# Optimization experiments

Measured on AMD Instinct MI355X. Metric: run time of the kernel, lower is better.

## Reference

```python
import jax, jax.numpy as jnp
import numpy as np

NUM_HEADS = 16


def setup_inputs() -> dict:
    key = jax.random.key(0)
    ks = jax.random.split(key, 5)
    B, S, D = 2, 2048, 1024
    x = jax.random.normal(ks[0], (B, S, D), dtype=jnp.float32)
    # Linear weights stored torch-style as [out, in]; init scale ~ 1/sqrt(D)
    scale = 1.0 / np.sqrt(D)
    Wq = jax.random.uniform(ks[1], (D, D), jnp.float32, -scale, scale)
    bq = jax.random.uniform(ks[2], (D,), jnp.float32, -scale, scale)
    Wo = jax.random.uniform(ks[3], (D, D), jnp.float32, -scale, scale)
    bo = jax.random.uniform(ks[4], (D,), jnp.float32, -scale, scale)
    return {"x": x, "Wq": Wq, "bq": bq, "Wo": Wo, "bo": bo}


def reference(x, Wq, bq, Wo, bo):
    B, S, D = x.shape
    H = NUM_HEADS
    Hd = D // H
    # NOTE: faithful to the source bug — Q, K, V all use the *query* projection.
    q = x @ Wq.T + bq                       # [B,S,D]
    qh = q.reshape(B, S, H, Hd).transpose(0, 2, 1, 3)  # [B,H,S,Hd]
    scores = jnp.einsum('bhsd,bhtd->bhst', qh, qh) / jnp.sqrt(jnp.float32(Hd))
    weights = jax.nn.softmax(scores, axis=-1)          # [B,H,S,S]
    attn = jnp.einsum('bhst,bhtd->bhsd', weights, qh)  # [B,H,S,Hd]
    attn = attn.transpose(0, 2, 1, 3).reshape(B, S, D)
    return attn @ Wo.T + bo
```

## Files before the change

### kernel.cpp

```cpp
#include <hip/hip_runtime.h>
#include <hip/hip_bf16.h>

typedef __bf16 bf16x8 __attribute__((ext_vector_type(8)));
typedef float  f32x4  __attribute__((ext_vector_type(4)));
typedef float  f32x16 __attribute__((ext_vector_type(16)));

__device__ __forceinline__ void gload_lds16(const void* g, void* l) {
  __builtin_amdgcn_global_load_lds(
      (const __attribute__((address_space(1))) unsigned int*)g,
      (__attribute__((address_space(3))) unsigned int*)l, 16, 0, 0);
}

__device__ __forceinline__ void xcd_remap(int& x, int& y) {
  const int lin = blockIdx.x + (blockIdx.y << 4);
  const int xcd = lin & 7, slot = lin >> 3;
  y = ((slot >> 4) << 3) + xcd;
  x = slot & 15;
}

__global__ void k_cvt(const float* __restrict__ s, __bf16* __restrict__ d, int n4) {
  int i = blockIdx.x * blockDim.x + threadIdx.x;
  if (i >= n4) return;
  float4 v = ((const float4*)s)[i];
  union { __bf16 h[4]; uint2 u; } o;
  o.h[0] = (__bf16)v.x; o.h[1] = (__bf16)v.y;
  o.h[2] = (__bf16)v.z; o.h[3] = (__bf16)v.w;
  ((uint2*)d)[i] = o.u;
}

template<bool OUT_BF16>
__global__ __launch_bounds__(256, 2)
void k_gemm_bt(const __bf16* __restrict__ A, const __bf16* __restrict__ B,
               const float* __restrict__ bias, void* __restrict__ C,
               int M, int N, int K) {
  __shared__ __align__(16) __bf16 At[4][128 * 32];
  __shared__ __align__(16) __bf16 Bt[4][64 * 32];
  const int tid  = threadIdx.x;
  const int lane = tid & 63;
  const int w    = tid >> 6;
  const int wr   = w >> 1, wc = w & 1;
  int bx, by; xcd_remap(bx, by);
  const int bm = by * 128, bn = bx * 64;

  f32x4 acc[4][2] = {};

  const __bf16* ga = A + (size_t)(bm + (tid >> 2)) * K + (tid & 3) * 8;
  const __bf16* gb = B + (size_t)(bn + (tid >> 2)) * K + (tid & 3) * 8;

#pragma unroll
  for (int p = 0; p < 2; ++p) {
    gload_lds16(ga + p * 32,                  &At[p][(w * 16) * 32]);
    gload_lds16(ga + p * 32 + (size_t)64 * K, &At[p][(64 + w * 16) * 32]);
    gload_lds16(gb + p * 32,                  &Bt[p][(w * 16) * 32]);
  }

  const int NIT = K / 32;
  for (int it = 0; it < NIT; ++it) {
    const int cur = it & 3;
    if (it + 2 < NIT) {
      const int nb = (it + 2) & 3;
      const int k2 = (it + 2) * 32;
      gload_lds16(ga + k2,                  &At[nb][(w * 16) * 32]);
      gload_lds16(ga + k2 + (size_t)64 * K, &At[nb][(64 + w * 16) * 32]);
      gload_lds16(gb + k2,                  &Bt[nb][(w * 16) * 32]);
      asm volatile("s_waitcnt vmcnt(6)" ::: "memory");
    } else if (it + 2 == NIT) {
      asm volatile("s_waitcnt vmcnt(3)" ::: "memory");
    } else {
      asm volatile("s_waitcnt vmcnt(0)" ::: "memory");
    }
    __builtin_amdgcn_s_barrier();
    __builtin_amdgcn_sched_barrier(0);

    bf16x8 a[4], b[2];
#pragma unroll
    for (int mt = 0; mt < 4; ++mt)
      a[mt] = *(const bf16x8*)&At[cur][(wr * 64 + mt * 16 + (lane & 15)) * 32 + (lane >> 4) * 8];
#pragma unroll
    for (int nt = 0; nt < 2; ++nt)
      b[nt] = *(const bf16x8*)&Bt[cur][(wc * 32 + nt * 16 + (lane & 15)) * 32 + (lane >> 4) * 8];
    __builtin_amdgcn_s_setprio(1);
#pragma unroll
    for (int mt = 0; mt < 4; ++mt)
#pragma unroll
      for (int nt = 0; nt < 2; ++nt)
        acc[mt][nt] = __builtin_amdgcn_mfma_f32_16x16x32_bf16(a[mt], b[nt], acc[mt][nt], 0, 0, 0);
    __builtin_amdgcn_s_setprio(0);
  }

#pragma unroll
  for (int nt = 0; nt < 2; ++nt) {
    const int col = bn + wc * 32 + nt * 16 + (lane & 15);
    const float bv = bias[col];
#pragma unroll
    for (int mt = 0; mt < 4; ++mt) {
#pragma unroll
      for (int r = 0; r < 4; ++r) {
        const int row = bm + wr * 64 + mt * 16 + (lane >> 4) * 4 + r;
        const float v = acc[mt][nt][r] + bv;
        if (OUT_BF16) ((__bf16*)C)[(size_t)row * N + col] = (__bf16)v;
        else          ((float*)C)[(size_t)row * N + col]  = v;
      }
    }
  }
}

#define SWZ2(row, col) ((row) * 64 + ((col) ^ (((((row) & 7) ^ ((row) >> 3)) & 7) << 3)))

#define ATTN_TILE(T, KB, VB)                                                  \
  {                                                                           \
    *(bf16x8*)&KB[SWZ2(2 * sm, c0)]     = v0;                                 \
    *(bf16x8*)&KB[SWZ2(2 * sm + 1, c0)] = v1;                                 \
    _Pragma("unroll")                                                         \
    for (int j = 0; j < 8; ++j) {                                             \
      union { __bf16 b[2]; unsigned u; } pk;                                  \
      pk.b[0] = v0[j]; pk.b[1] = v1[j];                                       \
      *(unsigned*)&VB[SWZ2(c0 + j, 2 * sm)] = pk.u;                           \
    }                                                                         \
    __syncthreads();                                                          \
    if ((T) < 31) {                                                           \
      v0 = *(const bf16x8*)&gsrc[(size_t)((T) + 1) * 64 * 1024];              \
      v1 = *(const bf16x8*)&gsrc[(size_t)((T) + 1) * 64 * 1024 + 1024];       \
    }                                                                         \
    f32x16 s[2] = {};                                                         \
    _Pragma("unroll")                                                         \
    for (int kvf = 0; kvf < 2; ++kvf) {                                       \
      __builtin_amdgcn_s_setprio(1);                                          \
      _Pragma("unroll")                                                       \
      for (int ks = 0; ks < 4; ++ks) {                                        \
        bf16x8 ka = *(const bf16x8*)&KB[SWZ2(kvf * 32 + l31, ks * 16 + h * 8)]; \
        s[kvf] = __builtin_amdgcn_mfma_f32_32x32x16_bf16(ka, qb[ks], s[kvf], 0, 0, 0); \
      }                                                                       \
      __builtin_amdgcn_s_setprio(0);                                          \
    }                                                                         \
    float ls0 = 0.f, ls1 = 0.f, ls2 = 0.f, ls3 = 0.f;                         \
    unsigned P[2][4][2];                                                      \
    _Pragma("unroll")                                                         \
    for (int kvf = 0; kvf < 2; ++kvf) {                                       \
      _Pragma("unroll")                                                       \
      for (int rq = 0; rq < 4; ++rq) {                                        \
        _Pragma("unroll")                                                     \
        for (int tt = 0; tt < 2; ++tt) {                                      \
          const float p0 = __builtin_amdgcn_exp2f(s[kvf][rq * 4 + tt * 2]);   \
          const float p1 = __builtin_amdgcn_exp2f(s[kvf][rq * 4 + tt * 2 + 1]); \
          if (tt == 0) { ls0 += p0; ls1 += p1; } else { ls2 += p0; ls3 += p1; } \
          union { __bf16 b[2]; unsigned u; } pk;                              \
          pk.b[0] = (__bf16)p0; pk.b[1] = (__bf16)p1;                         \
          P[kvf][rq][tt] = pk.u;                                              \
        }                                                                     \
      }                                                                       \
    }                                                                         \
    float lsum = (ls0 + ls1) + (ls2 + ls3);                                   \
    lsum += __shfl_xor(lsum, 32);                                             \
    l_run += lsum;                                                            \
    _Pragma("unroll")                                                         \
    for (int ko = 0; ko < 4; ++ko) {                                          \
      const int kvf = ko >> 1, rqa = (ko & 1) * 2, rqb = rqa + 1;             \
      asm volatile("v_permlane32_swap_b32 %0, %1"                             \
                   : "+v"(P[kvf][rqa][0]), "+v"(P[kvf][rqb][0]));             \
      asm volatile("v_permlane32_swap_b32 %0, %1"                             \
                   : "+v"(P[kvf][rqa][1]), "+v"(P[kvf][rqb][1]));             \
    }                                                                         \
    _Pragma("unroll")                                                         \
    for (int dh = 0; dh < 2; ++dh) {                                          \
      __builtin_amdgcn_s_setprio(1);                                          \
      _Pragma("unroll")                                                       \
      for (int ko = 0; ko < 4; ++ko) {                                        \
        const int kvf = ko >> 1, rqa = (ko & 1) * 2, rqb = rqa + 1;           \
        union { unsigned u[4]; bf16x8 v; } pu;                                \
        pu.u[0] = P[kvf][rqa][0]; pu.u[1] = P[kvf][rqa][1];                   \
        pu.u[2] = P[kvf][rqb][0]; pu.u[3] = P[kvf][rqb][1];                   \
        bf16x8 vb = *(const bf16x8*)&VB[SWZ2(dh * 32 + l31, ko * 16 + h * 8)]; \
        O[dh] = __builtin_amdgcn_mfma_f32_32x32x16_bf16(pu.v, vb, O[dh], 0, 0, 0); \
      }                                                                       \
      __builtin_amdgcn_s_setprio(0);                                          \
    }                                                                         \
  }

__global__ __launch_bounds__(256, 2)
void k_attn(const __bf16* __restrict__ q, __bf16* __restrict__ o) {
  __shared__ __align__(16) __bf16 Kt[2][64 * 64];
  __shared__ __align__(16) __bf16 Vt[2][64 * 64];
  const int tid = threadIdx.x, lane = tid & 63;
  const int w = tid >> 6;
  const int l31 = lane & 31, h = lane >> 5;
  int bqx, bh; xcd_remap(bqx, bh);
  const size_t base = ((size_t)(bh >> 4) * 2048) * 1024 + (bh & 15) * 64;
  const int q0 = bqx * 128 + w * 32;
  const float c2 = 0.18033688f;

  bf16x8 qb[4];
#pragma unroll
  for (int ks = 0; ks < 4; ++ks) {
    union { bf16x8 v; __bf16 b[8]; } u;
    u.v = *(const bf16x8*)&q[base + (size_t)(q0 + l31) * 1024 + ks * 16 + h * 8];
#pragma unroll
    for (int j = 0; j < 8; ++j) u.b[j] = (__bf16)((float)u.b[j] * c2);
    qb[ks] = u.v;
  }

  f32x16 O[2] = {};
  float l_run = 0.f;

  const int sm = tid >> 3, c0 = (tid & 7) * 8;
  const __bf16* gsrc = q + base + (size_t)(2 * sm) * 1024 + c0;

  __bf16* const K0 = &Kt[0][0];  __bf16* const V0 = &Vt[0][0];
  __bf16* const K1 = &Kt[1][0];  __bf16* const V1 = &Vt[1][0];

  bf16x8 v0 = *(const bf16x8*)&gsrc[0];
  bf16x8 v1 = *(const bf16x8*)&gsrc[1024];

  for (int t2 = 0; t2 < 16; ++t2) {
    ATTN_TILE(2 * t2,     K0, V0)
    ATTN_TILE(2 * t2 + 1, K1, V1)
  }

  const float linv = 1.0f / l_run;
#pragma unroll
  for (int r = 0; r < 16; ++r) {
    const int qrow = (r & 3) + 8 * (r >> 2) + 4 * h;
    const float rs = __shfl(linv, qrow);
    o[base + (size_t)(q0 + qrow) * 1024 + l31]      = (__bf16)(O[0][r] * rs);
    o[base + (size_t)(q0 + qrow) * 1024 + 32 + l31] = (__bf16)(O[1][r] * rs);
  }
}

extern "C" void kernel_launch(void* const* d_in, const int* in_sizes, int n_in,
                              void* d_out, int out_size, void* d_ws, size_t ws_size,
                              hipStream_t stream) {
  const float* x  = (const float*)d_in[0];
  const float* Wq = (const float*)d_in[1];
  const float* bq = (const float*)d_in[2];
  const float* Wo = (const float*)d_in[3];
  const float* bo = (const float*)d_in[4];

  char* ws = (char*)d_ws;
  __bf16* xb  = (__bf16*)(ws);
  __bf16* ab  = (__bf16*)(ws);
  __bf16* wqb = (__bf16*)(ws + ((size_t)8  << 20));
  __bf16* wob = (__bf16*)(ws + ((size_t)10 << 20));
  __bf16* qb  = (__bf16*)(ws + ((size_t)12 << 20));

  const int M = 4096, N = 1024, K = 1024;

  k_cvt<<<(M * K / 4 + 255) / 256, 256, 0, stream>>>(x,  xb,  M * K / 4);
  k_cvt<<<(N * K / 4 + 255) / 256, 256, 0, stream>>>(Wq, wqb, N * K / 4);
  k_cvt<<<(N * K / 4 + 255) / 256, 256, 0, stream>>>(Wo, wob, N * K / 4);

  k_gemm_bt<true ><<<dim3(16, 32), 256, 0, stream>>>(xb, wqb, bq, qb, M, N, K);
  k_attn          <<<dim3(16, 32), 256, 0, stream>>>(qb, ab);
  k_gemm_bt<false><<<dim3(16, 32), 256, 0, stream>>>(ab, wob, bo, d_out, M, N, K);
}
```

Before: 97.95 us.

## Split attention KV range across two blocks with merge kernel; deepen GEMM k-step

New measurement: 104.0 us. 1.06x slower.

```diff
diff --git a/kernel.cpp b/kernel.cpp
--- a/kernel.cpp
+++ b/kernel.cpp
@@ -33,8 +33,8 @@
 void k_gemm_bt(const __bf16* __restrict__ A, const __bf16* __restrict__ B,
                const float* __restrict__ bias, void* __restrict__ C,
                int M, int N, int K) {
-  __shared__ __align__(16) __bf16 At[4][128 * 32];
-  __shared__ __align__(16) __bf16 Bt[4][64 * 32];
+  __shared__ __align__(16) __bf16 At[3][2][128 * 32];
+  __shared__ __align__(16) __bf16 Bt[3][2][64 * 32];
   const int tid  = threadIdx.x;
   const int lane = tid & 63;
   const int w    = tid >> 6;
@@ -47,46 +47,56 @@
   const __bf16* ga = A + (size_t)(bm + (tid >> 2)) * K + (tid & 3) * 8;
   const __bf16* gb = B + (size_t)(bn + (tid >> 2)) * K + (tid & 3) * 8;
 
-#pragma unroll
-  for (int p = 0; p < 2; ++p) {
-    gload_lds16(ga + p * 32,                  &At[p][(w * 16) * 32]);
-    gload_lds16(ga + p * 32 + (size_t)64 * K, &At[p][(64 + w * 16) * 32]);
-    gload_lds16(gb + p * 32,                  &Bt[p][(w * 16) * 32]);
-  }
-
-  const int NIT = K / 32;
+#define STAGE_TILE(buf, k0)                                                     \
+  gload_lds16(ga + (k0),                       &At[buf][0][(w * 16) * 32]);     \
+  gload_lds16(ga + (k0) + (size_t)64 * K,      &At[buf][0][(64 + w * 16) * 32]);\
+  gload_lds16(ga + (k0) + 32,                  &At[buf][1][(w * 16) * 32]);     \
+  gload_lds16(ga + (k0) + 32 + (size_t)64 * K, &At[buf][1][(64 + w * 16) * 32]);\
+  gload_lds16(gb + (k0),                       &Bt[buf][0][(w * 16) * 32]);     \
+  gload_lds16(gb + (k0) + 32,                  &Bt[buf][1][(w * 16) * 32]);
+
+  STAGE_TILE(0, 0)
+  STAGE_TILE(1, 64)
+
+  const int NIT = K / 64;
   for (int it = 0; it < NIT; ++it) {
-    const int cur = it & 3;
+    const int cur = it % 3;
     if (it + 2 < NIT) {
-      const int nb = (it + 2) & 3;
-      const int k2 = (it + 2) * 32;
-      gload_lds16(ga + k2,                  &At[nb][(w * 16) * 32]);
-      gload_lds16(ga + k2 + (size_t)64 * K, &At[nb][(64 + w * 16) * 32]);
-      gload_lds16(gb + k2,                  &Bt[nb][(w * 16) * 32]);
       asm volatile("s_waitcnt vmcnt(6)" ::: "memory");
     } else if (it + 2 == NIT) {
-      asm volatile("s_waitcnt vmcnt(3)" ::: "memory");
+      asm volatile("s_waitcnt vmcnt(6)" ::: "memory");
     } else {
       asm volatile("s_waitcnt vmcnt(0)" ::: "memory");
     }
     __builtin_amdgcn_s_barrier();
     __builtin_amdgcn_sched_barrier(0);
-
-    bf16x8 a[4], b[2];
-#pragma unroll
-    for (int mt = 0; mt < 4; ++mt)
-      a[mt] = *(const bf16x8*)&At[cur][(wr * 64 + mt * 16 + (lane & 15)) * 32 + (lane >> 4) * 8];
-#pragma unroll
-    for (int nt = 0; nt < 2; ++nt)
-      b[nt] = *(const bf16x8*)&Bt[cur][(wc * 32 + nt * 16 + (lane & 15)) * 32 + (lane >> 4) * 8];
+    if (it + 2 < NIT) {
+      const int sb = (it + 2) % 3;
+      const int k2 = (it + 2) * 64;
+      STAGE_TILE(sb, k2)
+    }
+
+    bf16x8 a[2][4], b[2][2];
+#pragma unroll
+    for (int sl = 0; sl < 2; ++sl) {
+#pragma unroll
+      for (int mt = 0; mt < 4; ++mt)
+        a[sl][mt] = *(const bf16x8*)&At[cur][sl][(wr * 64 + mt * 16 + (lane & 15)) * 32 + (lane >> 4) * 8];
+#pragma unroll
+      for (int nt = 0; nt < 2; ++nt)
+        b[sl][nt] = *(const bf16x8*)&Bt[cur][sl][(wc * 32 + nt * 16 + (lane & 15)) * 32 + (lane >> 4) * 8];
+    }
     __builtin_amdgcn_s_setprio(1);
 #pragma unroll
-    for (int mt = 0; mt < 4; ++mt)
-#pragma unroll
-      for (int nt = 0; nt < 2; ++nt)
-        acc[mt][nt] = __builtin_amdgcn_mfma_f32_16x16x32_bf16(a[mt], b[nt], acc[mt][nt], 0, 0, 0);
+    for (int sl = 0; sl < 2; ++sl)
+#pragma unroll
+      for (int mt = 0; mt < 4; ++mt)
+#pragma unroll
+        for (int nt = 0; nt < 2; ++nt)
+          acc[mt][nt] = __builtin_amdgcn_mfma_f32_16x16x32_bf16(a[sl][mt], b[sl][nt], acc[mt][nt], 0, 0, 0);
     __builtin_amdgcn_s_setprio(0);
   }
+#undef STAGE_TILE
 
 #pragma unroll
   for (int nt = 0; nt < 2; ++nt) {
@@ -118,72 +128,65 @@
       *(unsigned*)&VB[SWZ2(c0 + j, 2 * sm)] = pk.u;                           \
     }                                                                         \
     __syncthreads();                                                          \
-    if ((T) < 31) {                                                           \
+    if ((T) < 15) {                                                           \
       v0 = *(const bf16x8*)&gsrc[(size_t)((T) + 1) * 64 * 1024];              \
       v1 = *(const bf16x8*)&gsrc[(size_t)((T) + 1) * 64 * 1024 + 1024];       \
     }                                                                         \
-    f32x16 s[2] = {};                                                         \
     _Pragma("unroll")                                                         \
     for (int kvf = 0; kvf < 2; ++kvf) {                                       \
+      f32x16 s = {};                                                          \
       __builtin_amdgcn_s_setprio(1);                                          \
       _Pragma("unroll")                                                       \
       for (int ks = 0; ks < 4; ++ks) {                                        \
         bf16x8 ka = *(const bf16x8*)&KB[SWZ2(kvf * 32 + l31, ks * 16 + h * 8)]; \
-        s[kvf] = __builtin_amdgcn_mfma_f32_32x32x16_bf16(ka, qb[ks], s[kvf], 0, 0, 0); \
+        s = __builtin_amdgcn_mfma_f32_32x32x16_bf16(ka, qb[ks], s, 0, 0, 0);  \
       }                                                                       \
       __builtin_amdgcn_s_setprio(0);                                          \
-    }                                                                         \
-    float ls0 = 0.f, ls1 = 0.f, ls2 = 0.f, ls3 = 0.f;                         \
-    unsigned P[2][4][2];                                                      \
-    _Pragma("unroll")                                                         \
-    for (int kvf = 0; kvf < 2; ++kvf) {                                       \
+      unsigned P[4][2];                                                       \
       _Pragma("unroll")                                                       \
       for (int rq = 0; rq < 4; ++rq) {                                        \
         _Pragma("unroll")                                                     \
         for (int tt = 0; tt < 2; ++tt) {                                      \
-          const float p0 = __builtin_amdgcn_exp2f(s[kvf][rq * 4 + tt * 2]);   \
-          const float p1 = __builtin_amdgcn_exp2f(s[kvf][rq * 4 + tt * 2 + 1]); \
+          const float p0 = __builtin_amdgcn_exp2f(s[rq * 4 + tt * 2]);        \
+          const float p1 = __builtin_amdgcn_exp2f(s[rq * 4 + tt * 2 + 1]);    \
           if (tt == 0) { ls0 += p0; ls1 += p1; } else { ls2 += p0; ls3 += p1; } \
           union { __bf16 b[2]; unsigned u; } pk;                              \
           pk.b[0] = (__bf16)p0; pk.b[1] = (__bf16)p1;                         \
-          P[kvf][rq][tt] = pk.u;                                              \
+          P[rq][tt] = pk.u;                                                   \
         }                                                                     \
       }                                                                       \
-    }                                                                         \
-    float lsum = (ls0 + ls1) + (ls2 + ls3);                                   \
-    lsum += __shfl_xor(lsum, 32);                                             \
-    l_run += lsum;                                                            \
-    _Pragma("unroll")                                                         \
-    for (int ko = 0; ko < 4; ++ko) {                                          \
-      const int kvf = ko >> 1, rqa = (ko & 1) * 2, rqb = rqa + 1;             \
-      asm volatile("v_permlane32_swap_b32 %0, %1"                             \
-                   : "+v"(P[kvf][rqa][0]), "+v"(P[kvf][rqb][0]));             \
-      asm volatile("v_permlane32_swap_b32 %0, %1"                             \
-                   : "+v"(P[kvf][rqa][1]), "+v"(P[kvf][rqb][1]));             \
-    }                                                                         \
-    _Pragma("unroll")                                                         \
-    for (int dh = 0; dh < 2; ++dh) {                                          \
+      _Pragma("unroll")                                                       \
+      for (int ko = 0; ko < 2; ++ko) {                                        \
+        asm volatile("v_permlane32_swap_b32 %0, %1"                           \
+                     : "+v"(P[ko * 2][0]), "+v"(P[ko * 2 + 1][0]));           \
+        asm volatile("v_permlane32_swap_b32 %0, %1"                           \
+                     : "+v"(P[ko * 2][1]), "+v"(P[ko * 2 + 1][1]));           \
+      }                                                                       \
       __builtin_amdgcn_s_setprio(1);                                          \
       _Pragma("unroll")                                                       \
-      for (int ko = 0; ko < 4; ++ko) {                                        \
-        const int kvf = ko >> 1, rqa = (ko & 1) * 2, rqb = rqa + 1;           \
-        union { unsigned u[4]; bf16x8 v; } pu;                                \
-        pu.u[0] = P[kvf][rqa][0]; pu.u[1] = P[kvf][rqa][1];                   \
-        pu.u[2] = P[kvf][rqb][0]; pu.u[3] = P[kvf][rqb][1];                   \
-        bf16x8 vb = *(const bf16x8*)&VB[SWZ2(dh * 32 + l31, ko * 16 + h * 8)]; \
-        O[dh] = __builtin_amdgcn_mfma_f32_32x32x16_bf16(pu.v, vb, O[dh], 0, 0, 0); \
+      for (int dh = 0; dh < 2; ++dh) {                                        \
+        _Pragma("unroll")                                                     \
+        for (int ko = 0; ko < 2; ++ko) {                                      \
+          union { unsigned u[4]; bf16x8 v; } pu;                              \
+          pu.u[0] = P[ko * 2][0];     pu.u[1] = P[ko * 2][1];                 \
+          pu.u[2] = P[ko * 2 + 1][0]; pu.u[3] = P[ko * 2 + 1][1];             \
+          bf16x8 vb = *(const bf16x8*)&VB[SWZ2(dh * 32 + l31, (kvf * 2 + ko) * 16 + h * 8)]; \
+          O[dh] = __builtin_amdgcn_mfma_f32_32x32x16_bf16(pu.v, vb, O[dh], 0, 0, 0); \
+        }                                                                     \
       }                                                                       \
       __builtin_amdgcn_s_setprio(0);                                          \
     }                                                                         \
   }
 
-__global__ __launch_bounds__(256, 2)
-void k_attn(const __bf16* __restrict__ q, __bf16* __restrict__ o) {
+__global__ __launch_bounds__(256, 4)
+void k_attn(const __bf16* __restrict__ q, __bf16* __restrict__ op,
+            float* __restrict__ ml) {
   __shared__ __align__(16) __bf16 Kt[2][64 * 64];
   __shared__ __align__(16) __bf16 Vt[2][64 * 64];
   const int tid = threadIdx.x, lane = tid & 63;
   const int w = tid >> 6;
   const int l31 = lane & 31, h = lane >> 5;
+  const int z = blockIdx.z;
   int bqx, bh; xcd_remap(bqx, bh);
   const size_t base = ((size_t)(bh >> 4) * 2048) * 1024 + (bh & 15) * 64;
   const int q0 = bqx * 128 + w * 32;
@@ -200,10 +203,10 @@
   }
 
   f32x16 O[2] = {};
-  float l_run = 0.f;
+  float ls0 = 0.f, ls1 = 0.f, ls2 = 0.f, ls3 = 0.f;
 
   const int sm = tid >> 3, c0 = (tid & 7) * 8;
-  const __bf16* gsrc = q + base + (size_t)(2 * sm) * 1024 + c0;
+  const __bf16* gsrc = q + base + (size_t)(z * 1024 + 2 * sm) * 1024 + c0;
 
   __bf16* const K0 = &Kt[0][0];  __bf16* const V0 = &Vt[0][0];
   __bf16* const K1 = &Kt[1][0];  __bf16* const V1 = &Vt[1][0];
@@ -211,19 +214,43 @@
   bf16x8 v0 = *(const bf16x8*)&gsrc[0];
   bf16x8 v1 = *(const bf16x8*)&gsrc[1024];
 
-  for (int t2 = 0; t2 < 16; ++t2) {
+  for (int t2 = 0; t2 < 8; ++t2) {
     ATTN_TILE(2 * t2,     K0, V0)
     ATTN_TILE(2 * t2 + 1, K1, V1)
   }
 
+  float l_run = (ls0 + ls1) + (ls2 + ls3);
+  l_run += __shfl_xor(l_run, 32);
   const float linv = 1.0f / l_run;
+  if (h == 0) ml[z * 65536 + bh * 2048 + (q0 + l31)] = l_run;
+  __bf16* opz = op + (size_t)z * 4194304;
 #pragma unroll
   for (int r = 0; r < 16; ++r) {
     const int qrow = (r & 3) + 8 * (r >> 2) + 4 * h;
     const float rs = __shfl(linv, qrow);
-    o[base + (size_t)(q0 + qrow) * 1024 + l31]      = (__bf16)(O[0][r] * rs);
-    o[base + (size_t)(q0 + qrow) * 1024 + 32 + l31] = (__bf16)(O[1][r] * rs);
-  }
+    opz[base + (size_t)(q0 + qrow) * 1024 + l31]      = (__bf16)(O[0][r] * rs);
+    opz[base + (size_t)(q0 + qrow) * 1024 + 32 + l31] = (__bf16)(O[1][r] * rs);
+  }
+}
+
+__global__ __launch_bounds__(256)
+void k_merge(const __bf16* __restrict__ op, const float* __restrict__ ml,
+             __bf16* __restrict__ out) {
+  const int idx = blockIdx.x * 256 + threadIdx.x;
+  const int d8 = idx & 7, hh = (idx >> 3) & 15, row = idx >> 7;
+  const int b = row >> 11, s = row & 2047;
+  const int mli = (b * 16 + hh) * 2048 + s;
+  const float lA = ml[mli], lB = ml[65536 + mli];
+  const float inv = 1.0f / (lA + lB);
+  const float fA = lA * inv, fB = lB * inv;
+  const size_t off = (size_t)row * 1024 + hh * 64 + d8 * 8;
+  bf16x8 a = *(const bf16x8*)&op[off];
+  bf16x8 c = *(const bf16x8*)&op[4194304 + off];
+  union { __bf16 h[8]; bf16x8 v; } r;
+#pragma unroll
+  for (int j = 0; j < 8; ++j)
+    r.h[j] = (__bf16)((float)a[j] * fA + (float)c[j] * fB);
+  *(bf16x8*)&out[off] = r.v;
 }
 
 extern "C" void kernel_launch(void* const* d_in, const int* in_sizes, int n_in,
@@ -236,11 +263,13 @@
   const float* bo = (const float*)d_in[4];
 
   char* ws = (char*)d_ws;
-  __bf16* xb  = (__bf16*)(ws);
-  __bf16* ab  = (__bf16*)(ws);
-  __bf16* wqb = (__bf16*)(ws + ((size_t)8  << 20));
-  __bf16* wob = (__bf16*)(ws + ((size_t)10 << 20));
-  __bf16* qb  = (__bf16*)(ws + ((size_t)12 << 20));
+  __bf16* xb    = (__bf16*)(ws);
+  __bf16* ab    = (__bf16*)(ws);
+  __bf16* wqb   = (__bf16*)(ws + ((size_t)8  << 20));
+  __bf16* wob   = (__bf16*)(ws + ((size_t)10 << 20));
+  __bf16* qb    = (__bf16*)(ws + ((size_t)12 << 20));
+  __bf16* opart = (__bf16*)(ws + ((size_t)20 << 20));
+  float*  mlbuf = (float*) (ws + ((size_t)36 << 20));
 
   const int M = 4096, N = 1024, K = 1024;
 
@@ -249,6 +278,7 @@
   k_cvt<<<(N * K / 4 + 255) / 256, 256, 0, stream>>>(Wo, wob, N * K / 4);
 
   k_gemm_bt<true ><<<dim3(16, 32), 256, 0, stream>>>(xb, wqb, bq, qb, M, N, K);
-  k_attn          <<<dim3(16, 32), 256, 0, stream>>>(qb, ab);
+  k_attn          <<<dim3(16, 32, 2), 256, 0, stream>>>(qb, opart, mlbuf);
+  k_merge         <<<2048, 256, 0, stream>>>(opart, mlbuf, ab);
   k_gemm_bt<false><<<dim3(16, 32), 256, 0, stream>>>(ab, wob, bo, d_out, M, N, K);
 }
```
